# Performance work log

Hardware: AMD Instinct MI355X
Metric: run time of the kernel (lower is better)

The kernel has to match this reference:

```python
import jax, jax.numpy as jnp
import numpy as np

B, T, E, D, A, V, EMB = 256, 64, 2048, 512, 512, 10000, 256

def _glorot(key, shape):
    lim = np.sqrt(6.0 / (shape[0] + shape[-1]))
    return jax.random.uniform(key, shape, jnp.float32, -lim, lim)

def setup_inputs() -> dict:
    key = jax.random.key(0)
    ks = jax.random.split(key, 16)
    return {
        'input_c': jax.random.randint(ks[0], (B, 1), 0, V),
        'hidden': jax.random.normal(ks[1], (B, D), jnp.float32),
        'carry': jax.random.normal(ks[2], (B, D), jnp.float32),
        'encoder_output': jax.random.normal(ks[3], (B, T, E), jnp.float32),
        'emb': jax.random.normal(ks[4], (V, EMB), jnp.float32) * 0.05,
        'w1': _glorot(ks[5], (D, A)),  'b1': jnp.zeros((A,), jnp.float32),
        'w2': _glorot(ks[6], (E, A)),  'b2': jnp.zeros((A,), jnp.float32),
        'v':  _glorot(ks[7], (A, 1)),  'bv': jnp.zeros((1,), jnp.float32),
        'wx': _glorot(ks[8], (E + EMB, 4 * D)),
        'wh': _glorot(ks[9], (D, 4 * D)),
        'bl': jnp.zeros((4 * D,), jnp.float32),
        'wp': _glorot(ks[10], (D, V)), 'bp': jnp.zeros((V,), jnp.float32),
    }

def reference(input_c, hidden, carry, encoder_output, emb, w1, b1, w2, b2, v, bv, wx, wh, bl, wp, bp):
    # embedding: [B,1] -> [B,EMB] after squeeze
    x = emb[input_c[:, 0]]
    # Bahdanau additive attention: score = v^T tanh(W1 h + W2 enc)
    q = hidden @ w1 + b1                                # [B,A]
    k = jnp.einsum('bte,ea->bta', encoder_output, w2) + b2  # [B,T,A]
    score = jnp.tanh(q[:, None, :] + k) @ v + bv        # [B,T,1]
    attn = jax.nn.softmax(score, axis=1)                # [B,T,1]
    context = jnp.sum(attn * encoder_output, axis=1)    # [B,E]
    # LSTM cell (keras gate order i,f,c,o); dropout inactive (training=False)
    lstm_in = jnp.concatenate([context, x], axis=-1)    # [B,E+EMB]
    z = lstm_in @ wx + hidden @ wh + bl                 # [B,4D]
    i, f, g, o = jnp.split(z, 4, axis=-1)
    c_new = jax.nn.sigmoid(f) * carry + jax.nn.sigmoid(i) * jnp.tanh(g)
    h_new = jax.nn.sigmoid(o) * jnp.tanh(c_new)
    logits = h_new @ wp + bp                            # [B,V]
    return logits, h_new, c_new
```

## Files before the change

kernel.cpp:

```cpp
#include <hip/hip_runtime.h>
#include <hip/hip_bf16.h>
#include <math.h>

#define BB 256
#define TT 64
#define EE 2048
#define DD 512
#define AA 512
#define VV 10000
#define VPAD 10240
#define EMBD 256
#define KLSTM (EE + EMBD + DD)
#define N4D (4 * DD)
#define MROWS (BB * TT)

using bf16x8 = __attribute__((ext_vector_type(8))) __bf16;
using f32x4  = __attribute__((ext_vector_type(4))) float;

__device__ __forceinline__ float sigf(float x) { return 1.f / (1.f + expf(-x)); }

__global__ void k_q(const float* __restrict__ hidden, const float* __restrict__ w1,
                    const float* __restrict__ b1, const float* __restrict__ b2,
                    float* __restrict__ qq) {
    __shared__ float hs[DD];
    const int b = blockIdx.x, tid = threadIdx.x;
    {
        float2 hv = *(const float2*)&hidden[(size_t)b * DD + 2 * tid];
        hs[2 * tid] = hv.x; hs[2 * tid + 1] = hv.y;
    }
    __syncthreads();
    const int a0 = 2 * tid;
    float2 acc = {0.f, 0.f};
    #pragma unroll 4
    for (int k = 0; k < DD; ++k) {
        float2 w = *(const float2*)&w1[(size_t)k * AA + a0];
        float h = hs[k];
        acc.x = fmaf(h, w.x, acc.x);
        acc.y = fmaf(h, w.y, acc.y);
    }
    qq[(size_t)b * AA + a0]     = acc.x + b1[a0]     + b2[a0];
    qq[(size_t)b * AA + a0 + 1] = acc.y + b1[a0 + 1] + b2[a0 + 1];
}

__global__ void k_w2t(const float* __restrict__ w2, __bf16* __restrict__ w2t) {
    __shared__ float t[32][33];
    const int k0 = blockIdx.x * 32, n0 = blockIdx.y * 32;
    const int tx = threadIdx.x, ty = threadIdx.y;
    #pragma unroll
    for (int i = 0; i < 4; ++i)
        t[ty + 8 * i][tx] = w2[(size_t)(k0 + ty + 8 * i) * AA + n0 + tx];
    __syncthreads();
    #pragma unroll
    for (int i = 0; i < 4; ++i)
        w2t[(size_t)(n0 + ty + 8 * i) * EE + k0 + tx] = (__bf16)t[tx][ty + 8 * i];
}

__global__ void k_wxht(const float* __restrict__ wx, const float* __restrict__ wh,
                       __bf16* __restrict__ wt) {
    __shared__ float t[32][33];
    const int k0 = blockIdx.x * 32, n0 = blockIdx.y * 32;
    const int tx = threadIdx.x, ty = threadIdx.y;
    #pragma unroll
    for (int i = 0; i < 4; ++i) {
        int k = k0 + ty + 8 * i;
        const float* wrow = (k < EE + EMBD) ? &wx[(size_t)k * N4D] : &wh[(size_t)(k - EE - EMBD) * N4D];
        t[ty + 8 * i][tx] = wrow[n0 + tx];
    }
    __syncthreads();
    #pragma unroll
    for (int i = 0; i < 4; ++i)
        wt[(size_t)(n0 + ty + 8 * i) * KLSTM + k0 + tx] = (__bf16)t[tx][ty + 8 * i];
}

__global__ void k_wpt(const float* __restrict__ wp, __bf16* __restrict__ wpt) {
    __shared__ float t[32][33];
    const int k0 = blockIdx.x * 32, n0 = blockIdx.y * 32;
    const int tx = threadIdx.x, ty = threadIdx.y;
    #pragma unroll
    for (int i = 0; i < 4; ++i) {
        int n = n0 + tx;
        t[ty + 8 * i][tx] = wp[(size_t)(k0 + ty + 8 * i) * VV + (n < VV ? n : VV - 1)];
    }
    __syncthreads();
    #pragma unroll
    for (int i = 0; i < 4; ++i)
        wpt[(size_t)(n0 + ty + 8 * i) * DD + k0 + tx] = (__bf16)t[tx][ty + 8 * i];
}

__global__ __launch_bounds__(512, 1) void k_attn(
        const float* __restrict__ enc, const __bf16* __restrict__ w2t,
        const float* __restrict__ qq, const float* __restrict__ vvec,
        const float* __restrict__ bv, float* __restrict__ attnG) {
    __shared__ bf16x8 Abuf[2][64][8];
    __shared__ float qs[AA], vs[AA];
    __shared__ float wred[8][64];
    const int b = blockIdx.x;
    const int tid = threadIdx.x;
    const int l = tid & 63, wv = tid >> 6;
    const int n0w = wv * 64;
    const int ar = l & 15, agr = l >> 4;

    qs[tid] = qq[(size_t)b * AA + tid];
    vs[tid] = vvec[tid];

    const int srow = tid >> 3, skseg = tid & 7;
    const float* encrow = enc + ((size_t)b * TT + srow) * EE + skseg * 8;
    const int sg = skseg ^ (srow & 7);

    const __bf16* bbase = w2t + (size_t)(n0w + ar) * EE + agr * 8;

    f32x4 acc[4][4];
    #pragma unroll
    for (int mi = 0; mi < 4; ++mi)
        #pragma unroll
        for (int ni = 0; ni < 4; ++ni)
            acc[mi][ni] = (f32x4){0.f, 0.f, 0.f, 0.f};

    {
        float4 u0 = *(const float4*)(encrow);
        float4 u1 = *(const float4*)(encrow + 4);
        bf16x8 pk;
        pk[0] = (__bf16)u0.x; pk[1] = (__bf16)u0.y; pk[2] = (__bf16)u0.z; pk[3] = (__bf16)u0.w;
        pk[4] = (__bf16)u1.x; pk[5] = (__bf16)u1.y; pk[6] = (__bf16)u1.z; pk[7] = (__bf16)u1.w;
        Abuf[0][srow][sg] = pk;
    }
    bf16x8 bA[8], bB[8];
    #pragma unroll
    for (int f = 0; f < 8; ++f)
        bA[f] = *(const bf16x8*)(bbase + (size_t)((f & 3) * 16) * EE + (f >> 2) * 32);
    __syncthreads();

    const int NIT = EE / 64;
    for (int itp = 0; itp < NIT / 2; ++itp) {
        const int it0 = 2 * itp, it1 = it0 + 1;

        #pragma unroll
        for (int f = 0; f < 8; ++f)
            bB[f] = *(const bf16x8*)(bbase + (size_t)((f & 3) * 16) * EE + it1 * 64 + (f >> 2) * 32);
        float4 p0 = *(const float4*)(encrow + it1 * 64);
        float4 p1 = *(const float4*)(encrow + it1 * 64 + 4);
        #pragma unroll
        for (int ks = 0; ks < 2; ++ks) {
            bf16x8 afr[4];
            #pragma unroll
            for (int mi = 0; mi < 4; ++mi)
                afr[mi] = Abuf[0][mi * 16 + ar][(ks * 4 + agr) ^ (ar & 7)];
            #pragma unroll
            for (int mi = 0; mi < 4; ++mi)
                #pragma unroll
                for (int ni = 0; ni < 4; ++ni)
                    acc[mi][ni] = __builtin_amdgcn_mfma_f32_16x16x32_bf16(afr[mi], bA[ks * 4 + ni], acc[mi][ni], 0, 0, 0);
        }
        {
            bf16x8 pk;
            pk[0] = (__bf16)p0.x; pk[1] = (__bf16)p0.y; pk[2] = (__bf16)p0.z; pk[3] = (__bf16)p0.w;
            pk[4] = (__bf16)p1.x; pk[5] = (__bf16)p1.y; pk[6] = (__bf16)p1.z; pk[7] = (__bf16)p1.w;
            Abuf[1][srow][sg] = pk;
        }
        __syncthreads();

        const bool more = (it1 + 1 < NIT);
        if (more) {
            #pragma unroll
            for (int f = 0; f < 8; ++f)
                bA[f] = *(const bf16x8*)(bbase + (size_t)((f & 3) * 16) * EE + (it1 + 1) * 64 + (f >> 2) * 32);
        }
        float4 q0, q1;
        if (more) {
            q0 = *(const float4*)(encrow + (it1 + 1) * 64);
            q1 = *(const float4*)(encrow + (it1 + 1) * 64 + 4);
        }
        #pragma unroll
        for (int ks = 0; ks < 2; ++ks) {
            bf16x8 afr[4];
            #pragma unroll
            for (int mi = 0; mi < 4; ++mi)
                afr[mi] = Abuf[1][mi * 16 + ar][(ks * 4 + agr) ^ (ar & 7)];
            #pragma unroll
            for (int mi = 0; mi < 4; ++mi)
                #pragma unroll
                for (int ni = 0; ni < 4; ++ni)
                    acc[mi][ni] = __builtin_amdgcn_mfma_f32_16x16x32_bf16(afr[mi], bB[ks * 4 + ni], acc[mi][ni], 0, 0, 0);
        }
        if (more) {
            bf16x8 pk;
            pk[0] = (__bf16)q0.x; pk[1] = (__bf16)q0.y; pk[2] = (__bf16)q0.z; pk[3] = (__bf16)q0.w;
            pk[4] = (__bf16)q1.x; pk[5] = (__bf16)q1.y; pk[6] = (__bf16)q1.z; pk[7] = (__bf16)q1.w;
            Abuf[0][srow][sg] = pk;
            __syncthreads();
        }
    }

    float sred[4][4];
    #pragma unroll
    for (int mi = 0; mi < 4; ++mi)
        #pragma unroll
        for (int r = 0; r < 4; ++r) sred[mi][r] = 0.f;
    #pragma unroll
    for (int ni = 0; ni < 4; ++ni) {
        const int col = n0w + ni * 16 + ar;
        const float qa = qs[col], va = vs[col];
        #pragma unroll
        for (int mi = 0; mi < 4; ++mi)
            #pragma unroll
            for (int r = 0; r < 4; ++r)
                sred[mi][r] += tanhf(qa + acc[mi][ni][r]) * va;
    }
    #pragma unroll
    for (int mi = 0; mi < 4; ++mi)
        #pragma unroll
        for (int r = 0; r < 4; ++r) {
            #pragma unroll
            for (int off = 1; off < 16; off <<= 1)
                sred[mi][r] += __shfl_xor(sred[mi][r], off, 64);
        }
    if (ar == 0) {
        #pragma unroll
        for (int mi = 0; mi < 4; ++mi)
            #pragma unroll
            for (int r = 0; r < 4; ++r)
                wred[wv][mi * 16 + agr * 4 + r] = sred[mi][r];
    }
    __syncthreads();
    if (tid < 64) {
        float s = bv[0];
        #pragma unroll
        for (int w = 0; w < 8; ++w) s += wred[w][tid];
        float mx = s;
        #pragma unroll
        for (int off = 1; off < 64; off <<= 1) mx = fmaxf(mx, __shfl_xor(mx, off, 64));
        float p = expf(s - mx);
        float sum = p;
        #pragma unroll
        for (int off = 1; off < 64; off <<= 1) sum += __shfl_xor(sum, off, 64);
        attnG[(size_t)b * TT + tid] = p / sum;
    }
}

__global__ void k_context(const float* __restrict__ enc, const float* __restrict__ attnG,
                          float* __restrict__ ctx) {
    __shared__ float attn[TT];
    const int b = blockIdx.y;
    const int tid = threadIdx.x;
    if (tid < 64) attn[tid] = attnG[(size_t)b * TT + tid];
    __syncthreads();
    const int e = blockIdx.x * 1024 + tid * 4;
    const float* encb = enc + (size_t)b * TT * EE + e;
    float4 acc = {0.f, 0.f, 0.f, 0.f};
    #pragma unroll 4
    for (int t = 0; t < TT; ++t) {
        float a = attn[t];
        float4 ev = *(const float4*)&encb[(size_t)t * EE];
        acc.x = fmaf(a, ev.x, acc.x);
        acc.y = fmaf(a, ev.y, acc.y);
        acc.z = fmaf(a, ev.z, acc.z);
        acc.w = fmaf(a, ev.w, acc.w);
    }
    *(float4*)&ctx[(size_t)b * EE + e] = acc;
}

#define ZKS 4
#define ZKC (KLSTM / ZKS)
#define ZNIT (ZKC / 32)
__global__ void k_z(const float* __restrict__ ctx, const float* __restrict__ emb,
                    const int* __restrict__ cidx, const float* __restrict__ hidden,
                    const __bf16* __restrict__ wt, float* __restrict__ zp) {
    __shared__ bf16x8 Abuf[32][ZKC / 8];
    __shared__ int cbs[32];
    const int tid = threadIdx.x;
    const int l = tid & 63, wv = tid >> 6;
    const int b0  = blockIdx.y * 32;
    const int kc0 = blockIdx.z * ZKC;
    const int nw  = blockIdx.x * 256 + wv * 64;

    if (tid < 32) cbs[tid] = cidx[b0 + tid];
    __syncthreads();

    {
        const int srow = tid >> 3, g0 = tid & 7;
        const int bg = b0 + srow;
        const int erow = cbs[srow];
        #pragma unroll
        for (int i = 0; i < 11; ++i) {
            int g = g0 + 8 * i;
            int k = kc0 + g * 8;
            const float* src;
            if (k < EE)             src = &ctx[(size_t)bg * EE + k];
            else if (k < EE + EMBD) src = &emb[(size_t)erow * EMBD + (k - EE)];
            else                    src = &hidden[(size_t)bg * DD + (k - EE - EMBD)];
            float4 u0 = *(const float4*)src;
            float4 u1 = *(const float4*)(src + 4);
            bf16x8 pk;
            pk[0] = (__bf16)u0.x; pk[1] = (__bf16)u0.y; pk[2] = (__bf16)u0.z; pk[3] = (__bf16)u0.w;
            pk[4] = (__bf16)u1.x; pk[5] = (__bf16)u1.y; pk[6] = (__bf16)u1.z; pk[7] = (__bf16)u1.w;
            Abuf[srow][g ^ (srow & 7)] = pk;
        }
    }
    __syncthreads();

    const int ar = l & 15, agr = l >> 4;
    const __bf16* bbase = wt + (size_t)(nw + ar) * KLSTM + kc0 + agr * 8;

    f32x4 acc[2][4];
    #pragma unroll
    for (int mt = 0; mt < 2; ++mt)
        #pragma unroll
        for (int f = 0; f < 4; ++f)
            acc[mt][f] = (f32x4){0.f, 0.f, 0.f, 0.f};

    bf16x8 bA[4], bBv[4];
    #pragma unroll
    for (int f = 0; f < 4; ++f)
        bA[f] = *(const bf16x8*)(bbase + (size_t)f * 16 * KLSTM);

    for (int itp = 0; itp < ZNIT / 2; ++itp) {
        const int it0 = 2 * itp, it1 = 2 * itp + 1;
        #pragma unroll
        for (int f = 0; f < 4; ++f)
            bBv[f] = *(const bf16x8*)(bbase + (size_t)f * 16 * KLSTM + it1 * 32);
        {
            bf16x8 a0 = Abuf[ar][(it0 * 4 + agr) ^ (ar & 7)];
            bf16x8 a1 = Abuf[16 + ar][(it0 * 4 + agr) ^ (ar & 7)];
            #pragma unroll
            for (int f = 0; f < 4; ++f) {
                acc[0][f] = __builtin_amdgcn_mfma_f32_16x16x32_bf16(a0, bA[f], acc[0][f], 0, 0, 0);
                acc[1][f] = __builtin_amdgcn_mfma_f32_16x16x32_bf16(a1, bA[f], acc[1][f], 0, 0, 0);
            }
        }
        const int it2 = (it1 + 1 < ZNIT) ? it1 + 1 : it1;
        #pragma unroll
        for (int f = 0; f < 4; ++f)
            bA[f] = *(const bf16x8*)(bbase + (size_t)f * 16 * KLSTM + it2 * 32);
        {
            bf16x8 a0 = Abuf[ar][(it1 * 4 + agr) ^ (ar & 7)];
            bf16x8 a1 = Abuf[16 + ar][(it1 * 4 + agr) ^ (ar & 7)];
            #pragma unroll
            for (int f = 0; f < 4; ++f) {
                acc[0][f] = __builtin_amdgcn_mfma_f32_16x16x32_bf16(a0, bBv[f], acc[0][f], 0, 0, 0);
                acc[1][f] = __builtin_amdgcn_mfma_f32_16x16x32_bf16(a1, bBv[f], acc[1][f], 0, 0, 0);
            }
        }
    }

    float* zpo = zp + (size_t)blockIdx.z * BB * N4D;
    #pragma unroll
    for (int mt = 0; mt < 2; ++mt)
        #pragma unroll
        for (int f = 0; f < 4; ++f)
            #pragma unroll
            for (int r = 0; r < 4; ++r)
                zpo[(size_t)(b0 + mt * 16 + agr * 4 + r) * N4D + nw + f * 16 + ar] = acc[mt][f][r];
}

__global__ void k_gates(const float* __restrict__ zp, const float* __restrict__ carry,
                        const float* __restrict__ bl,
                        float* __restrict__ hout, float* __restrict__ cout) {
    const int b = blockIdx.x, tid = threadIdx.x;
    const size_t P = (size_t)BB * N4D;
    #pragma unroll
    for (int r = 0; r < 2; ++r) {
        int d = tid + r * 256;
        float zi = bl[d], zf = bl[DD + d], zg = bl[2 * DD + d], zo = bl[3 * DD + d];
        #pragma unroll
        for (int ks = 0; ks < ZKS; ++ks) {
            const float* zb = zp + ks * P + (size_t)b * N4D;
            zi += zb[d];
            zf += zb[DD + d];
            zg += zb[2 * DD + d];
            zo += zb[3 * DD + d];
        }
        float c = carry[(size_t)b * DD + d];
        float cn = sigf(zf) * c + sigf(zi) * tanhf(zg);
        float hn = sigf(zo) * tanhf(cn);
        cout[(size_t)b * DD + d] = cn;
        hout[(size_t)b * DD + d] = hn;
    }
}

__global__ __launch_bounds__(256, 4) void k_logits(
        const float* __restrict__ hnew, const __bf16* __restrict__ wpt,
        const float* __restrict__ bp, float* __restrict__ logits) {
    __shared__ bf16x8 Abuf[64][8];
    __shared__ bf16x8 Bbuf[128][8];
    __shared__ float bps[128];
    const int tid = threadIdx.x;
    const int nb = blockIdx.x % 80, mb = blockIdx.x / 80;
    const int m0 = mb * 64, n0 = nb * 128;
    const int l = tid & 63, wv = tid >> 6;
    const int wm = wv >> 1, wn = wv & 1;
    const int ar = l & 15, agr = l >> 4;

    if (tid < 128) {
        int j = n0 + tid;
        bps[tid] = (j < VV) ? bp[j] : 0.f;
    }

    const int arow = tid >> 2, ag0 = (tid & 3) * 2;
    const float* aptr = hnew + (size_t)(m0 + arow) * DD + ag0 * 8;
    const int brow = tid >> 1, bg0 = (tid & 1) * 4;
    const __bf16* bptr = wpt + (size_t)(n0 + brow) * DD + bg0 * 8;

    f32x4 acc[2][4];
    #pragma unroll
    for (int mi = 0; mi < 2; ++mi)
        #pragma unroll
        for (int ni = 0; ni < 4; ++ni)
            acc[mi][ni] = (f32x4){0.f, 0.f, 0.f, 0.f};

    float4 af[4];
    bf16x8 bstg[4];
    #pragma unroll
    for (int j = 0; j < 4; ++j) af[j] = *(const float4*)(aptr + j * 4);
    #pragma unroll
    for (int i = 0; i < 4; ++i) bstg[i] = *(const bf16x8*)(bptr + i * 8);

    const int NIT = DD / 64;
    for (int it = 0; it < NIT; ++it) {
        if (it > 0) __syncthreads();
        {
            bf16x8 pk;
            pk[0] = (__bf16)af[0].x; pk[1] = (__bf16)af[0].y; pk[2] = (__bf16)af[0].z; pk[3] = (__bf16)af[0].w;
            pk[4] = (__bf16)af[1].x; pk[5] = (__bf16)af[1].y; pk[6] = (__bf16)af[1].z; pk[7] = (__bf16)af[1].w;
            Abuf[arow][ag0 ^ (arow & 7)] = pk;
            pk[0] = (__bf16)af[2].x; pk[1] = (__bf16)af[2].y; pk[2] = (__bf16)af[2].z; pk[3] = (__bf16)af[2].w;
            pk[4] = (__bf16)af[3].x; pk[5] = (__bf16)af[3].y; pk[6] = (__bf16)af[3].z; pk[7] = (__bf16)af[3].w;
            Abuf[arow][(ag0 + 1) ^ (arow & 7)] = pk;
        }
        #pragma unroll
        for (int i = 0; i < 4; ++i)
            Bbuf[brow][(bg0 + i) ^ (brow & 7)] = bstg[i];
        if (it + 1 < NIT) {
            const int k1 = (it + 1) * 64;
            #pragma unroll
            for (int j = 0; j < 4; ++j) af[j] = *(const float4*)(aptr + k1 + j * 4);
            #pragma unroll
            for (int i = 0; i < 4; ++i) bstg[i] = *(const bf16x8*)(bptr + k1 + i * 8);
        }
        __syncthreads();
        #pragma unroll
        for (int ks = 0; ks < 2; ++ks) {
            bf16x8 afr[2], bfr[4];
            #pragma unroll
            for (int mi = 0; mi < 2; ++mi)
                afr[mi] = Abuf[wm * 32 + mi * 16 + ar][(ks * 4 + agr) ^ (ar & 7)];
            #pragma unroll
            for (int ni = 0; ni < 4; ++ni)
                bfr[ni] = Bbuf[wn * 64 + ni * 16 + ar][(ks * 4 + agr) ^ (ar & 7)];
            #pragma unroll
            for (int mi = 0; mi < 2; ++mi)
                #pragma unroll
                for (int ni = 0; ni < 4; ++ni)
                    acc[mi][ni] = __builtin_amdgcn_mfma_f32_16x16x32_bf16(afr[mi], bfr[ni], acc[mi][ni], 0, 0, 0);
        }
    }

    #pragma unroll
    for (int mi = 0; mi < 2; ++mi)
        #pragma unroll
        for (int ni = 0; ni < 4; ++ni) {
            const int colL = wn * 64 + ni * 16 + ar;
            const int col = n0 + colL;
            if (col < VV) {
                const float bb = bps[colL];
                #pragma unroll
                for (int r = 0; r < 4; ++r) {
                    const int row = m0 + wm * 32 + mi * 16 + agr * 4 + r;
                    logits[(size_t)row * VV + col] = acc[mi][ni][r] + bb;
                }
            }
        }
}

extern "C" void kernel_launch(void* const* d_in, const int* in_sizes, int n_in,
                              void* d_out, int out_size, void* d_ws, size_t ws_size,
                              hipStream_t stream) {
    const int*   cidx   = (const int*)d_in[0];
    const float* hidden = (const float*)d_in[1];
    const float* carry  = (const float*)d_in[2];
    const float* enc    = (const float*)d_in[3];
    const float* emb    = (const float*)d_in[4];
    const float* w1     = (const float*)d_in[5];
    const float* b1     = (const float*)d_in[6];
    const float* w2     = (const float*)d_in[7];
    const float* b2     = (const float*)d_in[8];
    const float* vvec   = (const float*)d_in[9];
    const float* bv     = (const float*)d_in[10];
    const float* wx     = (const float*)d_in[11];
    const float* wh     = (const float*)d_in[12];
    const float* bl     = (const float*)d_in[13];
    const float* wp     = (const float*)d_in[14];
    const float* bp     = (const float*)d_in[15];

    float* out    = (float*)d_out;
    float* logits = out;
    float* hout   = out + (size_t)BB * VV;
    float* cout   = hout + (size_t)BB * DD;

    float* ws    = (float*)d_ws;
    float* qq    = ws;
    float* attnG = qq + (size_t)BB * AA;
    float* ctx   = attnG + (size_t)BB * TT;
    float* zp    = ctx + (size_t)BB * EE;
    __bf16* wxh_t = (__bf16*)(zp + (size_t)ZKS * BB * N4D);
    __bf16* wpt  = (__bf16*)(wxh_t + (size_t)N4D * KLSTM);
    __bf16* w2t  = (__bf16*)ctx;

    hipLaunchKernelGGL(k_w2t,     dim3(EE / 32, AA / 32),    dim3(32, 8), 0, stream, w2, w2t);
    hipLaunchKernelGGL(k_wxht,    dim3(KLSTM / 32, N4D / 32), dim3(32, 8), 0, stream, wx, wh, wxh_t);
    hipLaunchKernelGGL(k_wpt,     dim3(DD / 32, VPAD / 32),  dim3(32, 8), 0, stream, wp, wpt);
    hipLaunchKernelGGL(k_q,       dim3(BB),                  dim3(256), 0, stream, hidden, w1, b1, b2, qq);
    hipLaunchKernelGGL(k_attn,    dim3(BB),                  dim3(512), 0, stream, enc, w2t, qq, vvec, bv, attnG);
    hipLaunchKernelGGL(k_context, dim3(2, BB),               dim3(256), 0, stream, enc, attnG, ctx);
    hipLaunchKernelGGL(k_z,       dim3(N4D / 256, BB / 32, ZKS), dim3(256), 0, stream, ctx, emb, cidx, hidden, wxh_t, zp);
    hipLaunchKernelGGL(k_gates,   dim3(BB),                  dim3(256), 0, stream, zp, carry, bl, hout, cout);
    hipLaunchKernelGGL(k_logits,  dim3(320),                 dim3(256), 0, stream, hout, wpt, bp, logits);
}
```

Before: 195.1 us.

## Split attention score GEMM across two N-halves and fuse softmax into context kernel

The attention score kernel is restructured from one 512-thread block per batch row (all 512 A columns) into 512 blocks of 256 threads, each covering 64 rows and half of the A dimension. Each block writes partial scores, and the softmax moves into the context kernel, which sums the two partials before normalising. The aim is more blocks and higher occupancy (launch bounds 256,2) to fill the GPU's compute units better. In exchange, each encoder tile is loaded and converted twice (once per N-half), and an extra partial-score buffer round-trips through memory.

```diff
diff --git a/kernel.cpp b/kernel.cpp
--- a/kernel.cpp
+++ b/kernel.cpp
@@ -87,27 +87,26 @@
         wpt[(size_t)(n0 + ty + 8 * i) * DD + k0 + tx] = (__bf16)t[tx][ty + 8 * i];
 }
 
-__global__ __launch_bounds__(512, 1) void k_attn(
+__global__ __launch_bounds__(256, 2) void k_score(
         const float* __restrict__ enc, const __bf16* __restrict__ w2t,
         const float* __restrict__ qq, const float* __restrict__ vvec,
-        const float* __restrict__ bv, float* __restrict__ attnG) {
+        float* __restrict__ spart) {
     __shared__ bf16x8 Abuf[2][64][8];
-    __shared__ float qs[AA], vs[AA];
-    __shared__ float wred[8][64];
-    const int b = blockIdx.x;
+    __shared__ float qsv[256], vsv[256], wredL[4][64];
     const int tid = threadIdx.x;
+    const int mb = blockIdx.x & 255, nb = blockIdx.x >> 8;
+    const int m0 = mb * 64, n0 = nb * 256;
     const int l = tid & 63, wv = tid >> 6;
-    const int n0w = wv * 64;
+    const int nw = n0 + wv * 64;
     const int ar = l & 15, agr = l >> 4;
 
-    qs[tid] = qq[(size_t)b * AA + tid];
-    vs[tid] = vvec[tid];
-
-    const int srow = tid >> 3, skseg = tid & 7;
-    const float* encrow = enc + ((size_t)b * TT + srow) * EE + skseg * 8;
-    const int sg = skseg ^ (srow & 7);
-
-    const __bf16* bbase = w2t + (size_t)(n0w + ar) * EE + agr * 8;
+    qsv[tid] = qq[(size_t)mb * AA + n0 + tid];
+    vsv[tid] = vvec[n0 + tid];
+
+    const int arow = tid >> 2, ag0 = (tid & 3) * 2;
+    const float* aptr = enc + (size_t)(m0 + arow) * EE + ag0 * 8;
+
+    const __bf16* bbase = w2t + (size_t)(nw + ar) * EE + agr * 8;
 
     f32x4 acc[4][4];
     #pragma unroll
@@ -117,12 +116,17 @@
             acc[mi][ni] = (f32x4){0.f, 0.f, 0.f, 0.f};
 
     {
-        float4 u0 = *(const float4*)(encrow);
-        float4 u1 = *(const float4*)(encrow + 4);
+        float4 u0 = *(const float4*)(aptr);
+        float4 u1 = *(const float4*)(aptr + 4);
+        float4 u2 = *(const float4*)(aptr + 8);
+        float4 u3 = *(const float4*)(aptr + 12);
         bf16x8 pk;
         pk[0] = (__bf16)u0.x; pk[1] = (__bf16)u0.y; pk[2] = (__bf16)u0.z; pk[3] = (__bf16)u0.w;
         pk[4] = (__bf16)u1.x; pk[5] = (__bf16)u1.y; pk[6] = (__bf16)u1.z; pk[7] = (__bf16)u1.w;
-        Abuf[0][srow][sg] = pk;
+        Abuf[0][arow][ag0 ^ (arow & 7)] = pk;
+        pk[0] = (__bf16)u2.x; pk[1] = (__bf16)u2.y; pk[2] = (__bf16)u2.z; pk[3] = (__bf16)u2.w;
+        pk[4] = (__bf16)u3.x; pk[5] = (__bf16)u3.y; pk[6] = (__bf16)u3.z; pk[7] = (__bf16)u3.w;
+        Abuf[0][arow][(ag0 + 1) ^ (arow & 7)] = pk;
     }
     bf16x8 bA[8], bB[8];
     #pragma unroll
@@ -137,8 +141,10 @@
         #pragma unroll
         for (int f = 0; f < 8; ++f)
             bB[f] = *(const bf16x8*)(bbase + (size_t)((f & 3) * 16) * EE + it1 * 64 + (f >> 2) * 32);
-        float4 p0 = *(const float4*)(encrow + it1 * 64);
-        float4 p1 = *(const float4*)(encrow + it1 * 64 + 4);
+        float4 p0 = *(const float4*)(aptr + it1 * 64);
+        float4 p1 = *(const float4*)(aptr + it1 * 64 + 4);
+        float4 p2 = *(const float4*)(aptr + it1 * 64 + 8);
+        float4 p3 = *(const float4*)(aptr + it1 * 64 + 12);
         #pragma unroll
         for (int ks = 0; ks < 2; ++ks) {
             bf16x8 afr[4];
@@ -155,7 +161,10 @@
             bf16x8 pk;
             pk[0] = (__bf16)p0.x; pk[1] = (__bf16)p0.y; pk[2] = (__bf16)p0.z; pk[3] = (__bf16)p0.w;
             pk[4] = (__bf16)p1.x; pk[5] = (__bf16)p1.y; pk[6] = (__bf16)p1.z; pk[7] = (__bf16)p1.w;
-            Abuf[1][srow][sg] = pk;
+            Abuf[1][arow][ag0 ^ (arow & 7)] = pk;
+            pk[0] = (__bf16)p2.x; pk[1] = (__bf16)p2.y; pk[2] = (__bf16)p2.z; pk[3] = (__bf16)p2.w;
+            pk[4] = (__bf16)p3.x; pk[5] = (__bf16)p3.y; pk[6] = (__bf16)p3.z; pk[7] = (__bf16)p3.w;
+            Abuf[1][arow][(ag0 + 1) ^ (arow & 7)] = pk;
         }
         __syncthreads();
 
@@ -165,10 +174,12 @@
             for (int f = 0; f < 8; ++f)
                 bA[f] = *(const bf16x8*)(bbase + (size_t)((f & 3) * 16) * EE + (it1 + 1) * 64 + (f >> 2) * 32);
         }
-        float4 q0, q1;
+        float4 q0, q1, q2, q3;
         if (more) {
-            q0 = *(const float4*)(encrow + (it1 + 1) * 64);
-            q1 = *(const float4*)(encrow + (it1 + 1) * 64 + 4);
+            q0 = *(const float4*)(aptr + (it1 + 1) * 64);
+            q1 = *(const float4*)(aptr + (it1 + 1) * 64 + 4);
+            q2 = *(const float4*)(aptr + (it1 + 1) * 64 + 8);
+            q3 = *(const float4*)(aptr + (it1 + 1) * 64 + 12);
         }
         #pragma unroll
         for (int ks = 0; ks < 2; ++ks) {
@@ -186,7 +197,10 @@
             bf16x8 pk;
             pk[0] = (__bf16)q0.x; pk[1] = (__bf16)q0.y; pk[2] = (__bf16)q0.z; pk[3] = (__bf16)q0.w;
             pk[4] = (__bf16)q1.x; pk[5] = (__bf16)q1.y; pk[6] = (__bf16)q1.z; pk[7] = (__bf16)q1.w;
-            Abuf[0][srow][sg] = pk;
+            Abuf[0][arow][ag0 ^ (arow & 7)] = pk;
+            pk[0] = (__bf16)q2.x; pk[1] = (__bf16)q2.y; pk[2] = (__bf16)q2.z; pk[3] = (__bf16)q2.w;
+            pk[4] = (__bf16)q3.x; pk[5] = (__bf16)q3.y; pk[6] = (__bf16)q3.z; pk[7] = (__bf16)q3.w;
+            Abuf[0][arow][(ag0 + 1) ^ (arow & 7)] = pk;
             __syncthreads();
         }
     }
@@ -198,8 +212,8 @@
         for (int r = 0; r < 4; ++r) sred[mi][r] = 0.f;
     #pragma unroll
     for (int ni = 0; ni < 4; ++ni) {
-        const int col = n0w + ni * 16 + ar;
-        const float qa = qs[col], va = vs[col];
+        const int colL = wv * 64 + ni * 16 + ar;
+        const float qa = qsv[colL], va = vsv[colL];
         #pragma unroll
         for (int mi = 0; mi < 4; ++mi)
             #pragma unroll
@@ -219,13 +233,22 @@
         for (int mi = 0; mi < 4; ++mi)
             #pragma unroll
             for (int r = 0; r < 4; ++r)
-                wred[wv][mi * 16 + agr * 4 + r] = sred[mi][r];
-    }
-    __syncthreads();
+                wredL[wv][mi * 16 + agr * 4 + r] = sred[mi][r];
+    }
+    __syncthreads();
+    if (tid < 64)
+        spart[(size_t)nb * MROWS + m0 + tid] =
+            wredL[0][tid] + wredL[1][tid] + wredL[2][tid] + wredL[3][tid];
+}
+
+__global__ void k_context(const float* __restrict__ enc, const float* __restrict__ spart,
+                          const float* __restrict__ bv, float* __restrict__ ctx) {
+    __shared__ float attn[TT];
+    const int b = blockIdx.y;
+    const int tid = threadIdx.x;
     if (tid < 64) {
-        float s = bv[0];
-        #pragma unroll
-        for (int w = 0; w < 8; ++w) s += wred[w][tid];
+        const int m = b * TT + tid;
+        float s = spart[m] + spart[MROWS + m] + bv[0];
         float mx = s;
         #pragma unroll
         for (int off = 1; off < 64; off <<= 1) mx = fmaxf(mx, __shfl_xor(mx, off, 64));
@@ -233,16 +256,8 @@
         float sum = p;
         #pragma unroll
         for (int off = 1; off < 64; off <<= 1) sum += __shfl_xor(sum, off, 64);
-        attnG[(size_t)b * TT + tid] = p / sum;
-    }
-}
-
-__global__ void k_context(const float* __restrict__ enc, const float* __restrict__ attnG,
-                          float* __restrict__ ctx) {
-    __shared__ float attn[TT];
-    const int b = blockIdx.y;
-    const int tid = threadIdx.x;
-    if (tid < 64) attn[tid] = attnG[(size_t)b * TT + tid];
+        attn[tid] = p / sum;
+    }
     __syncthreads();
     const int e = blockIdx.x * 1024 + tid * 4;
     const float* encb = enc + (size_t)b * TT * EE + e;
@@ -498,19 +513,20 @@
 
     float* ws    = (float*)d_ws;
     float* qq    = ws;
-    float* attnG = qq + (size_t)BB * AA;
-    float* ctx   = attnG + (size_t)BB * TT;
+    float* score = qq + (size_t)BB * AA;
+    float* ctx   = score + (size_t)BB * TT;
     float* zp    = ctx + (size_t)BB * EE;
     __bf16* wxh_t = (__bf16*)(zp + (size_t)ZKS * BB * N4D);
-    __bf16* wpt  = (__bf16*)(wxh_t + (size_t)N4D * KLSTM);
+    float* spart = (float*)(wxh_t + (size_t)N4D * KLSTM);
+    __bf16* wpt  = (__bf16*)(spart + (size_t)4 * MROWS);
     __bf16* w2t  = (__bf16*)ctx;
 
     hipLaunchKernelGGL(k_w2t,     dim3(EE / 32, AA / 32),    dim3(32, 8), 0, stream, w2, w2t);
     hipLaunchKernelGGL(k_wxht,    dim3(KLSTM / 32, N4D / 32), dim3(32, 8), 0, stream, wx, wh, wxh_t);
     hipLaunchKernelGGL(k_wpt,     dim3(DD / 32, VPAD / 32),  dim3(32, 8), 0, stream, wp, wpt);
     hipLaunchKernelGGL(k_q,       dim3(BB),                  dim3(256), 0, stream, hidden, w1, b1, b2, qq);
-    hipLaunchKernelGGL(k_attn,    dim3(BB),                  dim3(512), 0, stream, enc, w2t, qq, vvec, bv, attnG);
-    hipLaunchKernelGGL(k_context, dim3(2, BB),               dim3(256), 0, stream, enc, attnG, ctx);
+    hipLaunchKernelGGL(k_score,   dim3(512),                 dim3(256), 0, stream, enc, w2t, qq, vvec, spart);
+    hipLaunchKernelGGL(k_context, dim3(2, BB),               dim3(256), 0, stream, enc, spart, bv, ctx);
     hipLaunchKernelGGL(k_z,       dim3(N4D / 256, BB / 32, ZKS), dim3(256), 0, stream, ctx, emb, cidx, hidden, wxh_t, zp);
     hipLaunchKernelGGL(k_gates,   dim3(BB),                  dim3(256), 0, stream, zp, carry, bl, hout, cout);
     hipLaunchKernelGGL(k_logits,  dim3(320),                 dim3(256), 0, stream, hout, wpt, bp, logits);
```

Measured after the change: 205.1 us. 1.05x slower.
